# Optimization experiments

Measured on AMD Instinct MI355X. Metric: run time of the kernel, lower is better.

Reference implementation:

```python
import jax, jax.numpy as jnp
import numpy as np

B, S, F, H, P = 2048, 168, 7, 128, 96  # batch, window, features, hidden, pred_len


def setup_inputs() -> dict:
    key = jax.random.key(0)
    ks = jax.random.split(key, 16)
    sc = 0.05
    return {
        "xb": jax.random.normal(ks[0], (B, S, F), dtype=jnp.float32),
        # encoder LSTM (1 layer, unidirectional); gate order i,f,g,o like torch
        "W_ih_enc": jax.random.normal(ks[1], (4 * H, F), dtype=jnp.float32) * sc,
        "W_hh_enc": jax.random.normal(ks[2], (4 * H, H), dtype=jnp.float32) * sc,
        "b_ih_enc": jax.random.normal(ks[3], (4 * H,), dtype=jnp.float32) * sc,
        "b_hh_enc": jax.random.normal(ks[4], (4 * H,), dtype=jnp.float32) * sc,
        # attention linear: (H+F) -> S
        "W_att": jax.random.normal(ks[5], (S, H + F), dtype=jnp.float32) * sc,
        "b_att": jax.random.normal(ks[6], (S,), dtype=jnp.float32) * sc,
        # decoder LSTMCell: input_size=H, hidden=H
        "W_ih_dec": jax.random.normal(ks[7], (4 * H, H), dtype=jnp.float32) * sc,
        "W_hh_dec": jax.random.normal(ks[8], (4 * H, H), dtype=jnp.float32) * sc,
        "b_ih_dec": jax.random.normal(ks[9], (4 * H,), dtype=jnp.float32) * sc,
        "b_hh_dec": jax.random.normal(ks[10], (4 * H,), dtype=jnp.float32) * sc,
        # out linear: H -> F
        "W_out": jax.random.normal(ks[11], (F, H), dtype=jnp.float32) * sc,
        "b_out": jax.random.normal(ks[12], (F,), dtype=jnp.float32) * sc,
        # final linear (output_size==1 branch): F -> 1
        "W_fin": jax.random.normal(ks[13], (1, F), dtype=jnp.float32) * sc,
        "b_fin": jax.random.normal(ks[14], (1,), dtype=jnp.float32) * sc,
    }


def _gates(pre):
    i, f, g, o = jnp.split(pre, 4, axis=-1)
    return jax.nn.sigmoid(i), jax.nn.sigmoid(f), jnp.tanh(g), jax.nn.sigmoid(o)


def _forward(xb, W_ih_enc, W_hh_enc, b_ih_enc, b_hh_enc, W_att, b_att,
             W_ih_dec, W_hh_dec, b_ih_dec, b_hh_dec, W_out, b_out, W_fin, b_fin):
    b_enc = b_ih_enc + b_hh_enc
    x_ih = jnp.einsum('bsf,gf->sbg', xb, W_ih_enc)  # precompute input projections [S,B,4H]

    def enc_step(carry, xg):
        h, c = carry
        i, f, g, o = _gates(xg + h @ W_hh_enc.T + b_enc)
        c = f * c + i * g
        h = o * jnp.tanh(c)
        return (h, c), h

    h0 = jnp.zeros((xb.shape[0], W_hh_enc.shape[1]), dtype=xb.dtype)
    (h_T, _), enc_hs = jax.lax.scan(enc_step, (h0, h0), x_ih)
    encoder_output = jnp.transpose(enc_hs, (1, 0, 2))  # [B,S,H]

    b_dec = b_ih_dec + b_hh_dec

    def dec_step(carry, _):
        prev_h, y_prev = carry
        attn_in = jnp.concatenate([prev_h, y_prev], axis=1)          # [B,H+F]
        attn_w = jax.nn.softmax(attn_in @ W_att.T + b_att, axis=-1)  # [B,S]
        combine = jnp.einsum('bs,bsh->bh', attn_w, encoder_output)   # [B,H]
        # torch code: rnn_hidden, rnn_hidden = cell(combine, (prev_h, prev_h))
        # -> the CELL state c' is what survives; h'/output gate discarded.
        i, f, g, _ = _gates(combine @ W_ih_dec.T + prev_h @ W_hh_dec.T + b_dec)
        c_new = f * prev_h + i * g
        out = c_new @ W_out.T + b_out                                # [B,F]
        return (c_new, out), out

    y0 = xb[:, -1, :]
    _, outs = jax.lax.scan(dec_step, (h_T, y0), None, length=P)      # [P,B,F]
    outputs = jnp.transpose(outs, (1, 0, 2))                         # [B,P,F]
    return outputs @ W_fin.T + b_fin                                 # [B,P,1]


def reference(xb, W_ih_enc, W_hh_enc, b_ih_enc, b_hh_enc, W_att, b_att,
              W_ih_dec, W_hh_dec, b_ih_dec, b_hh_dec, W_out, b_out, W_fin, b_fin):
    return _forward(xb, W_ih_enc, W_hh_enc, b_ih_enc, b_hh_enc, W_att, b_att,
                    W_ih_dec, W_hh_dec, b_ih_dec, b_hh_dec, W_out, b_out, W_fin, b_fin)
```

## Files before the change

kernel.cpp:

```cpp
#include <hip/hip_runtime.h>
#include <hip/hip_fp8.h>

#define NB   2048
#define SEQ  168
#define NF   7
#define NH   128
#define NP   96
#define EROWS 8
#define DROWS 8
#define NTHR 512
#define KE   160
#define KD   256
#define HXS  168
#define CTS  264
#define LS4  30

typedef _Float16 h16;
typedef _Float16 h16x8 __attribute__((ext_vector_type(8)));
typedef float    f32x2 __attribute__((ext_vector_type(2)));
typedef float    f32x4 __attribute__((ext_vector_type(4)));
typedef unsigned int u32x4 __attribute__((ext_vector_type(4)));

__device__ __forceinline__ void mfma_av(f32x4& acc, h16x8 a, const h16x8& b_agpr) {
  asm("v_mfma_f32_16x16x32_f16 %0, %1, %2, %0"
      : "+v"(acc) : "v"(a), "a"(b_agpr));
}
#define PIN_A(x) asm volatile("" : "+a"(x))

__device__ __forceinline__ float sigm(float x) { return 1.f / (1.f + __expf(-x)); }
__device__ __forceinline__ float tanh_(float x) {
  float e = __expf(-2.f * fabsf(x));
  return copysignf((1.f - e) / (1.f + e), x);
}

template <bool HI>
__device__ __forceinline__ unsigned int pack2_fp8(float a, float b, unsigned int old) {
#if __has_builtin(__builtin_amdgcn_cvt_pk_fp8_f32)
  return (unsigned int)__builtin_amdgcn_cvt_pk_fp8_f32(a, b, (int)old, HI);
#else
  __hip_fp8_e4m3 qa(a), qb(b);
  unsigned int pair = (unsigned int)(*(unsigned char*)&qa) |
                      ((unsigned int)(*(unsigned char*)&qb) << 8);
  return HI ? ((old & 0x0000ffffu) | (pair << 16)) : ((old & 0xffff0000u) | pair);
#endif
}
template <bool HI>
__device__ __forceinline__ f32x2 unp2(unsigned int w) {
#if __has_builtin(__builtin_amdgcn_cvt_pk_f32_fp8)
  return __builtin_amdgcn_cvt_pk_f32_fp8(w, HI);
#else
  __hip_fp8_e4m3 a, b;
  constexpr unsigned int sh = HI ? 16 : 0;
  *(unsigned char*)&a = (w >> sh) & 0xff;
  *(unsigned char*)&b = (w >> (sh + 8)) & 0xff;
  f32x2 r; r.x = (float)a; r.y = (float)b; return r;
#endif
}

constexpr size_t WENC_OFF   = 0;
constexpr size_t WDEC_OFF   = 163840;
constexpr size_t WEFF_OFF   = 425984;
constexpr size_t BEFF_OFF   = 468992;
constexpr size_t WCOMB_OFF  = 469760;
constexpr size_t BCONST_OFF = 470272;
constexpr size_t BENC_OFF   = 470528;
constexpr size_t BDEC_OFF   = 472576;
constexpr size_t ENC2_OFF   = 31981568;
constexpr size_t HT_OFF     = 44564480;

constexpr int HIST_OFF   = 0;
constexpr int CATH_OFF   = 122880;
constexpr int ATTW_OFF   = 131328;
constexpr int WAT2_OFF   = 136704;
constexpr int D0_OFF     = 146944;
constexpr int OUTP_OFF   = 152320;
constexpr int YH_OFF     = 152576;
constexpr int DPART_OFF  = 152832;
constexpr int DPART2_OFF = 153088;
constexpr int OBUF_OFF   = 153216;
constexpr int DSMEM      = 153472;
constexpr int SHHX_OFF = 122880;
constexpr int X16_OFF  = 133632;

__global__ void setup_weights(const float* __restrict__ Wih_enc, const float* __restrict__ Whh_enc,
                              const float* __restrict__ Wih_dec, const float* __restrict__ Whh_dec,
                              const float* __restrict__ Watt, const float* __restrict__ batt,
                              const float* __restrict__ Wout, const float* __restrict__ bout,
                              const float* __restrict__ Wfin, const float* __restrict__ bfin,
                              const float* __restrict__ bihe, const float* __restrict__ bhhe,
                              const float* __restrict__ bihd, const float* __restrict__ bhhd,
                              char* __restrict__ ws) {
  int idx = blockIdx.x * blockDim.x + threadIdx.x;
  constexpr int A0 = 81920;
  constexpr int A1 = A0 + 131072;
  constexpr int A2 = A1 + 21504;
  constexpr int A3 = A2 + 168;
  constexpr int A4 = A3 + 128;
  constexpr int A5 = A4 + 1;
  constexpr int A6 = A5 + 512;
  if (idx < A0) {
    int n = idx / KE, k = idx % KE;
    float v = 0.f;
    if (k < NF) v = Wih_enc[n * NF + k];
    else if (k >= 8 && k < 136) v = Whh_enc[n * NH + (k - 8)];
    ((h16*)(ws + WENC_OFF))[idx] = (h16)v;
  } else if (idx < A1) {
    int i = idx - A0;
    int n = i / KD, k = i % KD;
    float v = (k < NH) ? Wih_dec[n * NH + k] : Whh_dec[n * NH + (k - NH)];
    ((h16*)(ws + WDEC_OFF))[i] = (h16)v;
  } else if (idx < A2) {
    int i = idx - A1;
    int s = i / NH, k = i % NH;
    float v = Watt[s * (NH + NF) + k];
    #pragma unroll
    for (int f = 0; f < NF; ++f)
      v += Watt[s * (NH + NF) + NH + f] * Wout[f * NH + k];
    ((h16*)(ws + WEFF_OFF))[i] = (h16)v;
  } else if (idx < A3) {
    int s = idx - A2;
    float v = batt[s];
    #pragma unroll
    for (int f = 0; f < NF; ++f)
      v += Watt[s * (NH + NF) + NH + f] * bout[f];
    ((float*)(ws + BEFF_OFF))[s] = v;
  } else if (idx < A4) {
    int k = idx - A3;
    float v = 0.f;
    #pragma unroll
    for (int f = 0; f < NF; ++f) v += Wfin[f] * Wout[f * NH + k];
    ((float*)(ws + WCOMB_OFF))[k] = v;
  } else if (idx < A5) {
    float v = bfin[0];
    #pragma unroll
    for (int f = 0; f < NF; ++f) v += bout[f] * Wfin[f];
    ((float*)(ws + BCONST_OFF))[0] = v;
  } else if (idx < A6) {
    int g = idx - A5;
    ((float*)(ws + BENC_OFF))[g] = bihe[g] + bhhe[g];
    ((float*)(ws + BDEC_OFF))[g] = bihd[g] + bhhd[g];
  }
}

__global__ __attribute__((amdgpu_flat_work_group_size(NTHR, NTHR), amdgpu_waves_per_eu(2, 2)))
void fused_kernel(const float* __restrict__ xb, const h16* __restrict__ w16enc,
                  const float* __restrict__ bencp, unsigned int* __restrict__ encw2,
                  float* __restrict__ hTg,
                  const float* __restrict__ Watt, const float* __restrict__ Wout,
                  const float* __restrict__ bout,
                  const h16* __restrict__ w16dec, const h16* __restrict__ weff,
                  const float* __restrict__ beffp, const float* __restrict__ wcombp,
                  const float* __restrict__ bconstp, const float* __restrict__ bdecp,
                  float* __restrict__ out) {
  extern __shared__ char smem[];
  unsigned int* hist = (unsigned int*)(smem + HIST_OFF);
  h16 (*sh_hx)[16][HXS] = (h16(*)[16][HXS])(smem + SHHX_OFF);
  h16*   x16      = (h16*)(smem + X16_OFF);
  h16*   sh_cath  = (h16*)(smem + CATH_OFF);
  float* sh_attw  = (float*)(smem + ATTW_OFF);
  h16*   sh_watt2 = (h16*)(smem + WAT2_OFF);
  float* sh_d0    = (float*)(smem + D0_OFF);
  float* sh_outp  = (float*)(smem + OUTP_OFF);
  float* sh_yh    = (float*)(smem + YH_OFF);
  float* sh_dp    = (float*)(smem + DPART_OFF);
  float* sh_dp2   = (float*)(smem + DPART2_OFF);
  float* sh_obuf  = (float*)(smem + OBUF_OFF);

  const int t  = threadIdx.x;
  const int r0 = blockIdx.x * EROWS;

  const int w  = t >> 6;
  const int l  = t & 63;
  const int lq = l >> 4;
  const int ln = l & 15;
  const int hcol = w * 16 + ln;
  const int mrow = lq * 4;
  const bool act = (lq < 2);

  for (int i = t; i < 2 * 16 * HXS; i += NTHR) ((h16*)sh_hx)[i] = (h16)0.f;
  for (int i = t; i < EROWS * SEQ * NF; i += NTHR)
    x16[i] = (h16)xb[(size_t)r0 * SEQ * NF + i];

  h16x8 bfE[4][5];
  float bE[4];
  #pragma unroll
  for (int g = 0; g < 4; ++g) {
    int n = g * 128 + hcol;
    bE[g] = bencp[n];
    #pragma unroll
    for (int kt = 0; kt < 5; ++kt) {
      bfE[g][kt] = *(const h16x8*)(w16enc + n * KE + kt * 32 + lq * 8);
      PIN_A(bfE[g][kt]);
    }
  }
  __syncthreads();
  if (t < EROWS * NF) {
    int r = t / NF, f = t - (t / NF) * NF;
    sh_hx[0][r][f] = x16[(r * SEQ + 0) * NF + f];
  }

  float creg[4] = {0.f, 0.f, 0.f, 0.f};
  float hstate[4] = {0.f, 0.f, 0.f, 0.f};
  float hprev[4] = {0.f, 0.f, 0.f, 0.f};
  unsigned int hpack[4] = {0u, 0u, 0u, 0u};

  __syncthreads();

  for (int s = 0; s < SEQ; ++s) {
    const int cur = s & 1;

    f32x4 ac[4] = {{0.f,0.f,0.f,0.f},{0.f,0.f,0.f,0.f},{0.f,0.f,0.f,0.f},{0.f,0.f,0.f,0.f}};
    #pragma unroll
    for (int kt = 0; kt < 5; ++kt) {
      h16x8 af = *(const h16x8*)(&sh_hx[cur][ln][kt * 32 + lq * 8]);
      #pragma unroll
      for (int g = 0; g < 4; ++g)
        mfma_av(ac[g], af, bfE[g][kt]);
    }

    if (act) {
      #pragma unroll
      for (int reg = 0; reg < 4; ++reg) {
        float gi = sigm(ac[0][reg] + bE[0]);
        float gf = sigm(ac[1][reg] + bE[1]);
        float gg = tanh_(ac[2][reg] + bE[2]);
        float go = sigm(ac[3][reg] + bE[3]);
        float c = gf * creg[reg] + gi * gg;
        creg[reg] = c;
        float h = go * tanh_(c);
        hstate[reg] = h;
        sh_hx[cur ^ 1][mrow + reg][8 + hcol] = (h16)h;
        float hs = h * 16.f;
        if ((s & 1) == 0) hprev[reg] = hs;
        else if ((s & 3) == 1) hpack[reg] = pack2_fp8<false>(hprev[reg], hs, hpack[reg]);
        else                   hpack[reg] = pack2_fp8<true>(hprev[reg], hs, hpack[reg]);
      }
      if ((s & 3) == 3) {
        int s4 = s >> 2;
        if (s4 < LS4) {
          #pragma unroll
          for (int reg = 0; reg < 4; ++reg)
            hist[(size_t)(mrow + reg) * (LS4 * NH) + s4 * NH + hcol] = hpack[reg];
        } else {
          int q = s4 - LS4;
          #pragma unroll
          for (int reg = 0; reg < 4; ++reg)
            encw2[(((size_t)(r0 + mrow + reg) * 3 + (q >> 2)) * NH + hcol) * 4 + (q & 3)] = hpack[reg];
        }
      }
    }
    if (t < EROWS * NF && s + 1 < SEQ) {
      int r = t / NF, f = t - (t / NF) * NF;
      sh_hx[cur ^ 1][r][f] = x16[(r * SEQ + (s + 1)) * NF + f];
    }
    __syncthreads();
  }

  if (act) {
    #pragma unroll
    for (int reg = 0; reg < 4; ++reg)
      hTg[(size_t)(r0 + mrow + reg) * NH + hcol] = hstate[reg];
  }
  __builtin_amdgcn_sched_barrier(0);
  __syncthreads();

  for (int i = t; i < 40 * NH; i += NTHR) sh_watt2[i] = weff[128 * NH + i];
  if (t < 32) sh_dp2[t] = 0.f;

  h16x8 bfD[3][8];
  float bD[3];
  #pragma unroll
  for (int g = 0; g < 3; ++g) {
    int n = g * 128 + hcol;
    bD[g] = bdecp[n];
    #pragma unroll
    for (int kt = 0; kt < 8; ++kt) {
      bfD[g][kt] = *(const h16x8*)(w16dec + n * KD + kt * 32 + lq * 8);
      PIN_A(bfD[g][kt]);
    }
  }
  h16x8 bfA[4];
  #pragma unroll
  for (int kt = 0; kt < 4; ++kt) {
    bfA[kt] = *(const h16x8*)(weff + hcol * NH + kt * 32 + lq * 8);
    PIN_A(bfA[kt]);
  }
  const float beffR = beffp[hcol];
  const int s2v = 128 + hcol;
  const float beff2 = (w < 3 && s2v < SEQ) ? beffp[s2v] : 0.f;
  const float wcombR = wcombp[hcol];
  const float bconstv = bconstp[0];

  if (act) {
    #pragma unroll
    for (int reg = 0; reg < 4; ++reg) {
      creg[reg] = hstate[reg];
      sh_cath[0 * 8 * CTS + (mrow + reg) * CTS + 128 + hcol] = (h16)hstate[reg];
    }
  }
  if (t < DROWS * NF) {
    int r = t / NF, f = t - (t / NF) * NF;
    float a = bout[f];
    const float* wr = Wout + f * NH;
    const float* hp = hTg + (size_t)(r0 + r) * NH;
    #pragma unroll 8
    for (int k = 0; k < NH; k += 4) {
      float4 pv = *(const float4*)(hp + k);
      float4 wv = *(const float4*)(wr + k);
      a += pv.x * wv.x + pv.y * wv.y + pv.z * wv.z + pv.w * wv.w;
    }
    sh_yh[t] = a;
  }
  __syncthreads();
  for (int i = t; i < DROWS * SEQ; i += NTHR) {
    int r = i / SEQ, s = i - (i / SEQ) * SEQ;
    float a = 0.f;
    #pragma unroll
    for (int f = 0; f < NF; ++f) {
      float y0f = xb[((size_t)(r0 + r) * SEQ + (SEQ - 1)) * NF + f];
      a += (y0f - sh_yh[r * NF + f]) * Watt[s * (NH + NF) + NH + f];
    }
    sh_d0[i] = a;
  }

  const int dr = t >> 7;
  const int dh = t & 127;
  const unsigned int* hrowA = hist + (size_t)dr * (LS4 * NH) + dh;
  const unsigned int* hrowB = hist + (size_t)(dr + 4) * (LS4 * NH) + dh;
  const float* erowA = sh_attw + dr * SEQ;
  const float* erowB = sh_attw + (dr + 4) * SEQ;

  u32x4 tA[3], tB[3];
  {
    const u32x4* e2 = (const u32x4*)encw2;
    #pragma unroll
    for (int b = 0; b < 3; ++b) {
      tA[b] = e2[((size_t)(r0 + dr)     * 3 + b) * NH + dh];
      tB[b] = e2[((size_t)(r0 + dr + 4) * 3 + b) * NH + dh];
    }
  }
  __syncthreads();

  f32x4 aghh[3];

  for (int p = 0; p < NP; ++p) {
    const int CA = p & 1;

    if (p > 0 && t < DROWS) {
      float a = bconstv;
      #pragma unroll
      for (int w2 = 0; w2 < 8; ++w2) a += sh_outp[w2 * 8 + t];
      int slot = (p - 1) & 7;
      sh_obuf[t * 8 + slot] = a;
      if (slot == 7) {
        int base = p - 8;
        #pragma unroll
        for (int j = 0; j < 8; ++j)
          out[(size_t)(r0 + t) * NP + base + j] = sh_obuf[t * 8 + j];
      }
    }

    {
      h16x8 afA[4];
      #pragma unroll
      for (int kt = 0; kt < 4; ++kt)
        afA[kt] = *(const h16x8*)(sh_cath + CA * 8 * CTS + (ln & 7) * CTS + 128 + kt * 32 + lq * 8);
      f32x4 acc = {0.f, 0.f, 0.f, 0.f};
      #pragma unroll
      for (int kt = 0; kt < 4; ++kt)
        mfma_av(acc, afA[kt], bfA[kt]);
      #pragma unroll
      for (int g = 0; g < 3; ++g) {
        f32x4 z = {0.f, 0.f, 0.f, 0.f};
        aghh[g] = z;
        #pragma unroll
        for (int kt = 0; kt < 4; ++kt)
          mfma_av(aghh[g], afA[kt], bfD[g][4 + kt]);
      }

      float ev[4];
      if (act) {
        #pragma unroll
        for (int reg = 0; reg < 4; ++reg) {
          int row = mrow + reg;
          float lg = acc[reg] + beffR;
          if (p == 0) lg += sh_d0[row * SEQ + hcol];
          lg = fminf(fmaxf(lg, -30.f), 30.f);
          ev[reg] = __expf(lg);
          sh_attw[row * SEQ + hcol] = ev[reg];
        }
        #pragma unroll
        for (int reg = 0; reg < 4; ++reg) {
          float rs = ev[reg];
          rs += __shfl_xor(rs, 1);
          rs += __shfl_xor(rs, 2);
          rs += __shfl_xor(rs, 4);
          rs += __shfl_xor(rs, 8);
          if (ln == 0) sh_dp[(mrow + reg) * 8 + w] = rs;
        }
      }
      if (w < 3) {
        int srow = (s2v < SEQ ? s2v : SEQ - 1) - 128;
        f32x4 acc2 = {0.f, 0.f, 0.f, 0.f};
        #pragma unroll
        for (int kt = 0; kt < 4; ++kt) {
          h16x8 bf2 = *(const h16x8*)(sh_watt2 + srow * NH + kt * 32 + lq * 8);
          acc2 = __builtin_amdgcn_mfma_f32_16x16x32_f16(afA[kt], bf2, acc2, 0, 0, 0);
        }
        if (act) {
          float ev2[4];
          #pragma unroll
          for (int reg = 0; reg < 4; ++reg) {
            int row = mrow + reg;
            float e2v = 0.f;
            if (s2v < SEQ) {
              float lg = acc2[reg] + beff2;
              if (p == 0) lg += sh_d0[row * SEQ + s2v];
              lg = fminf(fmaxf(lg, -30.f), 30.f);
              e2v = __expf(lg);
              sh_attw[row * SEQ + s2v] = e2v;
            }
            ev2[reg] = e2v;
          }
          #pragma unroll
          for (int reg = 0; reg < 4; ++reg) {
            float rs = ev2[reg];
            rs += __shfl_xor(rs, 1);
            rs += __shfl_xor(rs, 2);
            rs += __shfl_xor(rs, 4);
            rs += __shfl_xor(rs, 8);
            if (ln == 0) sh_dp2[(mrow + reg) * 4 + w] = rs;
          }
        }
      }
    }
    __syncthreads();

    {
      float4 qa0 = *(const float4*)(sh_dp + dr * 8);
      float4 qa1 = *(const float4*)(sh_dp + dr * 8 + 4);
      float4 qa2 = *(const float4*)(sh_dp2 + dr * 4);
      float4 qb0 = *(const float4*)(sh_dp + (dr + 4) * 8);
      float4 qb1 = *(const float4*)(sh_dp + (dr + 4) * 8 + 4);
      float4 qb2 = *(const float4*)(sh_dp2 + (dr + 4) * 4);
      float dA = ((qa0.x + qa0.y) + (qa0.z + qa0.w)) + ((qa1.x + qa1.y) + (qa1.z + qa1.w))
               + ((qa2.x + qa2.y) + (qa2.z + qa2.w));
      float dB = ((qb0.x + qb0.y) + (qb0.z + qb0.w)) + ((qb1.x + qb1.y) + (qb1.z + qb1.w))
               + ((qb2.x + qb2.y) + (qb2.z + qb2.w));
      const float invA = 0.0625f / dA;
      const float invB = 0.0625f / dB;

      f32x2 avA = {0.f, 0.f};
      f32x2 avB = {0.f, 0.f};
      #pragma unroll 6
      for (int s4 = 0; s4 < LS4; ++s4) {
        unsigned int evA = hrowA[s4 * NH];
        unsigned int evB = hrowB[s4 * NH];
        float4 eA = *(const float4*)(erowA + s4 * 4);
        float4 eB = *(const float4*)(erowB + s4 * 4);
        f32x2 wA01 = {eA.x, eA.y}, wA23 = {eA.z, eA.w};
        f32x2 wB01 = {eB.x, eB.y}, wB23 = {eB.z, eB.w};
        avA = wA01 * unp2<false>(evA) + avA;
        avA = wA23 * unp2<true>(evA) + avA;
        avB = wB01 * unp2<false>(evB) + avB;
        avB = wB23 * unp2<true>(evB) + avB;
      }
      #pragma unroll
      for (int b = 0; b < 3; ++b) {
        #pragma unroll
        for (int jj = 0; jj < 4; ++jj) {
          int s4 = LS4 + b * 4 + jj;
          unsigned int evA = tA[b][jj];
          unsigned int evB = tB[b][jj];
          float4 eA = *(const float4*)(erowA + s4 * 4);
          float4 eB = *(const float4*)(erowB + s4 * 4);
          f32x2 wA01 = {eA.x, eA.y}, wA23 = {eA.z, eA.w};
          f32x2 wB01 = {eB.x, eB.y}, wB23 = {eB.z, eB.w};
          avA = wA01 * unp2<false>(evA) + avA;
          avA = wA23 * unp2<true>(evA) + avA;
          avB = wB01 * unp2<false>(evB) + avB;
          avB = wB23 * unp2<true>(evB) + avB;
        }
      }
      sh_cath[CA * 8 * CTS + dr * CTS + dh]       = (h16)((avA.x + avA.y) * invA);
      sh_cath[CA * 8 * CTS + (dr + 4) * CTS + dh] = (h16)((avB.x + avB.y) * invB);
    }
    __syncthreads();

    {
      f32x4 ag[3] = {aghh[0], aghh[1], aghh[2]};
      #pragma unroll
      for (int kt = 0; kt < 4; ++kt) {
        h16x8 af = *(const h16x8*)(sh_cath + CA * 8 * CTS + (ln & 7) * CTS + kt * 32 + lq * 8);
        #pragma unroll
        for (int g = 0; g < 3; ++g)
          mfma_av(ag[g], af, bfD[g][kt]);
      }
      if (act) {
        float contrib[4];
        #pragma unroll
        for (int reg = 0; reg < 4; ++reg) {
          int row = mrow + reg;
          float gi = sigm(ag[0][reg] + bD[0]);
          float gf = sigm(ag[1][reg] + bD[1]);
          float gg = tanh_(ag[2][reg] + bD[2]);
          float cn = gf * creg[reg] + gi * gg;
          creg[reg] = cn;
          sh_cath[(CA ^ 1) * 8 * CTS + row * CTS + 128 + hcol] = (h16)cn;
          contrib[reg] = cn * wcombR;
        }
        #pragma unroll
        for (int reg = 0; reg < 4; ++reg) {
          float rsum = contrib[reg];
          rsum += __shfl_xor(rsum, 1);
          rsum += __shfl_xor(rsum, 2);
          rsum += __shfl_xor(rsum, 4);
          rsum += __shfl_xor(rsum, 8);
          if (ln == 0) sh_outp[w * 8 + mrow + reg] = rsum;
        }
      }
    }
    __syncthreads();
  }

  if (t < DROWS) {
    float a = bconstv;
    #pragma unroll
    for (int w2 = 0; w2 < 8; ++w2) a += sh_outp[w2 * 8 + t];
    sh_obuf[t * 8 + 7] = a;
    #pragma unroll
    for (int j = 0; j < 8; ++j)
      out[(size_t)(r0 + t) * NP + (NP - 8) + j] = sh_obuf[t * 8 + j];
  }
}

extern "C" void kernel_launch(void* const* d_in, const int* in_sizes, int n_in,
                              void* d_out, int out_size, void* d_ws, size_t ws_size,
                              hipStream_t stream) {
  const float* xb      = (const float*)d_in[0];
  const float* Wih_enc = (const float*)d_in[1];
  const float* Whh_enc = (const float*)d_in[2];
  const float* bih_enc = (const float*)d_in[3];
  const float* bhh_enc = (const float*)d_in[4];
  const float* Watt    = (const float*)d_in[5];
  const float* batt    = (const float*)d_in[6];
  const float* Wih_dec = (const float*)d_in[7];
  const float* Whh_dec = (const float*)d_in[8];
  const float* bih_dec = (const float*)d_in[9];
  const float* bhh_dec = (const float*)d_in[10];
  const float* Wout    = (const float*)d_in[11];
  const float* bout    = (const float*)d_in[12];
  const float* Wfin    = (const float*)d_in[13];
  const float* bfin    = (const float*)d_in[14];
  char* ws = (char*)d_ws;

  hipFuncSetAttribute(reinterpret_cast<const void*>(fused_kernel),
                      hipFuncAttributeMaxDynamicSharedMemorySize, DSMEM);

  setup_weights<<<920, 256, 0, stream>>>(Wih_enc, Whh_enc, Wih_dec, Whh_dec,
                                         Watt, batt, Wout, bout, Wfin, bfin,
                                         bih_enc, bhh_enc, bih_dec, bhh_dec, ws);
  fused_kernel<<<NB / EROWS, NTHR, DSMEM, stream>>>(
      xb, (const h16*)(ws + WENC_OFF), (const float*)(ws + BENC_OFF),
      (unsigned int*)(ws + ENC2_OFF), (float*)(ws + HT_OFF),
      Watt, Wout, bout,
      (const h16*)(ws + WDEC_OFF), (const h16*)(ws + WEFF_OFF),
      (const float*)(ws + BEFF_OFF), (const float*)(ws + WCOMB_OFF),
      (const float*)(ws + BCONST_OFF), (const float*)(ws + BDEC_OFF),
      (float*)d_out);
}
```

Before: 996.0 us.

## Stream encoder inputs from global via register stash; keep final hidden in LDS

Drops the up-front staging of the whole input window into a shared-memory x16 buffer. Each of 224 threads now loads one future timestep every four steps into a register and writes it into the ping-pong input tile when its turn comes. The final encoder hidden state goes to shared memory instead of a global workspace round trip, so the output-projection init reads LDS. The decoder's h-part gate MFMAs are also moved from the early attention phase into a single 8-k-tile loop after the combine step. This frees LDS and global traffic but adds per-step global loads on the serial encoder path, and may lengthen the decoder's critical section.

```diff
diff --git a/kernel.cpp b/kernel.cpp
--- a/kernel.cpp
+++ b/kernel.cpp
@@ -66,7 +66,6 @@
 constexpr size_t BENC_OFF   = 470528;
 constexpr size_t BDEC_OFF   = 472576;
 constexpr size_t ENC2_OFF   = 31981568;
-constexpr size_t HT_OFF     = 44564480;
 
 constexpr int HIST_OFF   = 0;
 constexpr int CATH_OFF   = 122880;
@@ -75,12 +74,11 @@
 constexpr int D0_OFF     = 146944;
 constexpr int OUTP_OFF   = 152320;
 constexpr int YH_OFF     = 152576;
-constexpr int DPART_OFF  = 152832;
-constexpr int DPART2_OFF = 153088;
-constexpr int OBUF_OFF   = 153216;
+constexpr int OBUF_OFF   = 152832;
+constexpr int DPART_OFF  = 153088;
+constexpr int DPART2_OFF = 153344;
 constexpr int DSMEM      = 153472;
 constexpr int SHHX_OFF = 122880;
-constexpr int X16_OFF  = 133632;
 
 __global__ void setup_weights(const float* __restrict__ Wih_enc, const float* __restrict__ Whh_enc,
                               const float* __restrict__ Wih_dec, const float* __restrict__ Whh_dec,
@@ -145,7 +143,6 @@
 __global__ __attribute__((amdgpu_flat_work_group_size(NTHR, NTHR), amdgpu_waves_per_eu(2, 2)))
 void fused_kernel(const float* __restrict__ xb, const h16* __restrict__ w16enc,
                   const float* __restrict__ bencp, unsigned int* __restrict__ encw2,
-                  float* __restrict__ hTg,
                   const float* __restrict__ Watt, const float* __restrict__ Wout,
                   const float* __restrict__ bout,
                   const h16* __restrict__ w16dec, const h16* __restrict__ weff,
@@ -155,16 +152,15 @@
   extern __shared__ char smem[];
   unsigned int* hist = (unsigned int*)(smem + HIST_OFF);
   h16 (*sh_hx)[16][HXS] = (h16(*)[16][HXS])(smem + SHHX_OFF);
-  h16*   x16      = (h16*)(smem + X16_OFF);
   h16*   sh_cath  = (h16*)(smem + CATH_OFF);
   float* sh_attw  = (float*)(smem + ATTW_OFF);
   h16*   sh_watt2 = (h16*)(smem + WAT2_OFF);
   float* sh_d0    = (float*)(smem + D0_OFF);
   float* sh_outp  = (float*)(smem + OUTP_OFF);
   float* sh_yh    = (float*)(smem + YH_OFF);
+  float* sh_obuf  = (float*)(smem + OBUF_OFF);
   float* sh_dp    = (float*)(smem + DPART_OFF);
   float* sh_dp2   = (float*)(smem + DPART2_OFF);
-  float* sh_obuf  = (float*)(smem + OBUF_OFF);
 
   const int t  = threadIdx.x;
   const int r0 = blockIdx.x * EROWS;
@@ -177,9 +173,12 @@
   const int mrow = lq * 4;
   const bool act = (lq < 2);
 
+  const int j  = t & 3;
+  const int rf = t >> 2;
+  const int xr = rf / NF;
+  const int xf = rf - xr * NF;
+
   for (int i = t; i < 2 * 16 * HXS; i += NTHR) ((h16*)sh_hx)[i] = (h16)0.f;
-  for (int i = t; i < EROWS * SEQ * NF; i += NTHR)
-    x16[i] = (h16)xb[(size_t)r0 * SEQ * NF + i];
 
   h16x8 bfE[4][5];
   float bE[4];
@@ -196,18 +195,23 @@
   __syncthreads();
   if (t < EROWS * NF) {
     int r = t / NF, f = t - (t / NF) * NF;
-    sh_hx[0][r][f] = x16[(r * SEQ + 0) * NF + f];
+    sh_hx[0][r][f] = (h16)xb[((size_t)(r0 + r) * SEQ + 0) * NF + f];
   }
 
   float creg[4] = {0.f, 0.f, 0.f, 0.f};
   float hstate[4] = {0.f, 0.f, 0.f, 0.f};
   float hprev[4] = {0.f, 0.f, 0.f, 0.f};
   unsigned int hpack[4] = {0u, 0u, 0u, 0u};
+  float xstash = 0.f;
 
   __syncthreads();
 
   for (int s = 0; s < SEQ; ++s) {
     const int cur = s & 1;
+    if ((s & 3) == 0 && t < EROWS * NF * 4) {
+      int sx = s + 1 + j;
+      xstash = (sx < SEQ) ? xb[((size_t)(r0 + xr) * SEQ + sx) * NF + xf] : 0.f;
+    }
 
     f32x4 ac[4] = {{0.f,0.f,0.f,0.f},{0.f,0.f,0.f,0.f},{0.f,0.f,0.f,0.f},{0.f,0.f,0.f,0.f}};
     #pragma unroll
@@ -249,19 +253,16 @@
         }
       }
     }
-    if (t < EROWS * NF && s + 1 < SEQ) {
-      int r = t / NF, f = t - (t / NF) * NF;
-      sh_hx[cur ^ 1][r][f] = x16[(r * SEQ + (s + 1)) * NF + f];
-    }
+    if (t < EROWS * NF * 4 && (s & 3) == j && s + 1 < SEQ)
+      sh_hx[cur ^ 1][xr][xf] = (h16)xstash;
     __syncthreads();
   }
 
   if (act) {
     #pragma unroll
     for (int reg = 0; reg < 4; ++reg)
-      hTg[(size_t)(r0 + mrow + reg) * NH + hcol] = hstate[reg];
-  }
-  __builtin_amdgcn_sched_barrier(0);
+      sh_attw[(mrow + reg) * SEQ + hcol] = hstate[reg];
+  }
   __syncthreads();
 
   for (int i = t; i < 40 * NH; i += NTHR) sh_watt2[i] = weff[128 * NH + i];
@@ -302,7 +303,7 @@
     int r = t / NF, f = t - (t / NF) * NF;
     float a = bout[f];
     const float* wr = Wout + f * NH;
-    const float* hp = hTg + (size_t)(r0 + r) * NH;
+    const float* hp = sh_attw + r * SEQ;
     #pragma unroll 8
     for (int k = 0; k < NH; k += 4) {
       float4 pv = *(const float4*)(hp + k);
@@ -341,8 +342,6 @@
   }
   __syncthreads();
 
-  f32x4 aghh[3];
-
   for (int p = 0; p < NP; ++p) {
     const int CA = p & 1;
 
@@ -355,8 +354,8 @@
       if (slot == 7) {
         int base = p - 8;
         #pragma unroll
-        for (int j = 0; j < 8; ++j)
-          out[(size_t)(r0 + t) * NP + base + j] = sh_obuf[t * 8 + j];
+        for (int jj = 0; jj < 8; ++jj)
+          out[(size_t)(r0 + t) * NP + base + jj] = sh_obuf[t * 8 + jj];
       }
     }
 
@@ -369,17 +368,8 @@
       #pragma unroll
       for (int kt = 0; kt < 4; ++kt)
         mfma_av(acc, afA[kt], bfA[kt]);
-      #pragma unroll
-      for (int g = 0; g < 3; ++g) {
-        f32x4 z = {0.f, 0.f, 0.f, 0.f};
-        aghh[g] = z;
-        #pragma unroll
-        for (int kt = 0; kt < 4; ++kt)
-          mfma_av(aghh[g], afA[kt], bfD[g][4 + kt]);
-      }
-
-      float ev[4];
       if (act) {
+        float ev[4];
         #pragma unroll
         for (int reg = 0; reg < 4; ++reg) {
           int row = mrow + reg;
@@ -488,9 +478,9 @@
     __syncthreads();
 
     {
-      f32x4 ag[3] = {aghh[0], aghh[1], aghh[2]};
-      #pragma unroll
-      for (int kt = 0; kt < 4; ++kt) {
+      f32x4 ag[3] = {{0.f,0.f,0.f,0.f},{0.f,0.f,0.f,0.f},{0.f,0.f,0.f,0.f}};
+      #pragma unroll
+      for (int kt = 0; kt < 8; ++kt) {
         h16x8 af = *(const h16x8*)(sh_cath + CA * 8 * CTS + (ln & 7) * CTS + kt * 32 + lq * 8);
         #pragma unroll
         for (int g = 0; g < 3; ++g)
@@ -529,8 +519,8 @@
     for (int w2 = 0; w2 < 8; ++w2) a += sh_outp[w2 * 8 + t];
     sh_obuf[t * 8 + 7] = a;
     #pragma unroll
-    for (int j = 0; j < 8; ++j)
-      out[(size_t)(r0 + t) * NP + (NP - 8) + j] = sh_obuf[t * 8 + j];
+    for (int jj = 0; jj < 8; ++jj)
+      out[(size_t)(r0 + t) * NP + (NP - 8) + jj] = sh_obuf[t * 8 + jj];
   }
 }
 
@@ -562,7 +552,7 @@
                                          bih_enc, bhh_enc, bih_dec, bhh_dec, ws);
   fused_kernel<<<NB / EROWS, NTHR, DSMEM, stream>>>(
       xb, (const h16*)(ws + WENC_OFF), (const float*)(ws + BENC_OFF),
-      (unsigned int*)(ws + ENC2_OFF), (float*)(ws + HT_OFF),
+      (unsigned int*)(ws + ENC2_OFF),
       Watt, Wout, bout,
       (const h16*)(ws + WDEC_OFF), (const h16*)(ws + WEFF_OFF),
       (const float*)(ws + BEFF_OFF), (const float*)(ws + WCOMB_OFF),
```

New measurement: 1.003 ms. Within noise of the previous version (+0.7%).
